# Optimization experiments

Hardware: AMD Instinct MI355X
Metric: run time of the kernel (lower is better)

## Reference

```python
import jax, jax.numpy as jnp
import numpy as np

N_HEADS = 16
HEAD_DIM = 64
ROPE_BASE = 10000.0


def _apply_rope(x, offset):
    # x: (B, T, H, hd); rotates consecutive pairs (x[2i], x[2i+1]) as complex numbers,
    # matching torch.view_as_complex on reshape(..., -1, 2).
    B, T, H, hd = x.shape
    inv_freq = 1.0 / (ROPE_BASE ** (jnp.arange(0, hd, 2, dtype=jnp.float32) / hd))  # (hd/2,)
    t = jnp.arange(T, dtype=jnp.float32) + offset
    ang = t[:, None] * inv_freq[None, :]                      # (T, hd/2)
    cos = jnp.cos(ang)[None, :, None, :]                      # (1, T, 1, hd/2)
    sin = jnp.sin(ang)[None, :, None, :]
    x1 = x[..., 0::2]
    x2 = x[..., 1::2]
    out = jnp.stack([x1 * cos - x2 * sin, x1 * sin + x2 * cos], axis=-1)
    return out.reshape(B, T, H, hd).astype(x.dtype)


def setup_inputs() -> dict:
    key = jax.random.key(0)
    ks = jax.random.split(key, 5)
    D = N_HEADS * HEAD_DIM  # 1024
    s = 1.0 / np.sqrt(D)
    x = jax.random.normal(ks[0], (2, 2048, D), jnp.float32)
    Wqkv = jax.random.normal(ks[1], (D, 3 * D), jnp.float32) * s
    bqkv = jax.random.normal(ks[2], (3 * D,), jnp.float32) * 0.01
    Wout = jax.random.normal(ks[3], (D, D), jnp.float32) * s
    bout = jax.random.normal(ks[4], (D,), jnp.float32) * 0.01
    return {"x": x, "Wqkv": Wqkv, "bqkv": bqkv, "Wout": Wout, "bout": bout, "offset": 0}


def reference(x, Wqkv, bqkv, Wout, bout, offset):
    B, T, D = x.shape
    qkv = (x @ Wqkv + bqkv).reshape(B, T, 3, N_HEADS, HEAD_DIM)
    q, k, v = qkv[:, :, 0], qkv[:, :, 1], qkv[:, :, 2]       # (B, T, H, hd)
    q = _apply_rope(q, offset)
    k = _apply_rope(k, offset)
    # kv_cache is None and T == window_size, so no crop occurs.
    new_cache = jnp.stack([k, v], axis=1)                     # (B, 2, T, H, hd)
    scale = 1.0 / np.sqrt(HEAD_DIM)
    scores = jnp.einsum("bqhd,bkhd->bhqk", q, k) * scale      # (B, H, T, T)
    mask = jnp.tril(jnp.ones((T, T), dtype=bool))
    scores = jnp.where(mask[None, None], scores, jnp.finfo(scores.dtype).min)
    attn = jax.nn.softmax(scores, axis=-1)
    ctx = jnp.einsum("bhqk,bkhd->bqhd", attn, v).reshape(B, T, D)
    out = ctx @ Wout + bout
    return (out, new_cache)
```

## Files before the change

kernel.cpp:

```cpp
#include <hip/hip_runtime.h>
#include <stdint.h>
#include <math.h>


typedef __bf16 bf16_t;
typedef bf16_t bf16x8 __attribute__((ext_vector_type(8)));
typedef float f32x4 __attribute__((ext_vector_type(4)));
typedef unsigned short ushort8_t __attribute__((ext_vector_type(8)));

__device__ __forceinline__ unsigned short f2bf(float f) {
    union { float f; unsigned int i; } v; v.f = f;
    unsigned int r = v.i + 0x7fffu + ((v.i >> 16) & 1u);
    return (unsigned short)(r >> 16);
}
__device__ __forceinline__ bf16x8 ld8(const unsigned short* p) {
    return *(const bf16x8*)p;
}
__device__ __forceinline__ void gload_lds16(const unsigned short* g, unsigned short* l) {
    __builtin_amdgcn_global_load_lds(
        (__attribute__((address_space(1))) void*)(g),
        (__attribute__((address_space(3))) void*)(l),
        16, 0, 0);
}

__global__ void k_cvt(const float* __restrict__ in, unsigned short* __restrict__ out) {
    const int i = (blockIdx.x * 256 + threadIdx.x) * 8;
    float4 a = *(const float4*)&in[i];
    float4 b = *(const float4*)&in[i + 4];
    ushort8_t v;
    v[0] = f2bf(a.x); v[1] = f2bf(a.y); v[2] = f2bf(a.z); v[3] = f2bf(a.w);
    v[4] = f2bf(b.x); v[5] = f2bf(b.y); v[6] = f2bf(b.z); v[7] = f2bf(b.w);
    *(ushort8_t*)&out[i] = v;
}

__global__ void k_ropetab(float* __restrict__ tab, const int* __restrict__ offp) {
    int idx = blockIdx.x * blockDim.x + threadIdx.x;
    int t = idx >> 5, i = idx & 31;
    float off = (float)(*offp);
    float inv = powf(10000.0f, -(float)(2 * i) / 64.0f);
    float ang = ((float)t + off) * inv;
    float s, c;
    sincosf(ang, &s, &c);
    tab[idx * 2]     = c;
    tab[idx * 2 + 1] = s;
}

__global__ void k_transposeF2B(const float* __restrict__ in,
                               unsigned short* __restrict__ out, int R, int C) {
    __shared__ __align__(16) float tile[64 * 68];
    const int bz = blockIdx.z;
    const size_t base = (size_t)bz * R * C;
    const int tR = blockIdx.y * 64, tC = blockIdx.x * 64;
    const int tid = threadIdx.x;
#pragma unroll
    for (int it = 0; it < 4; ++it) {
        int flat = (it * 256 + tid) * 4;
        int r = flat >> 6, c = flat & 63;
        *(float4*)&tile[r * 68 + c] =
            *(const float4*)&in[base + (size_t)(tR + r) * C + tC + c];
    }
    __syncthreads();
#pragma unroll
    for (int it = 0; it < 2; ++it) {
        int flat = (it * 256 + tid) * 8;
        int rr = flat >> 6, cc = flat & 63;
        ushort8_t v;
#pragma unroll
        for (int j = 0; j < 8; ++j) v[j] = f2bf(tile[(cc + j) * 68 + rr]);
        *(ushort8_t*)&out[base + (size_t)(tC + rr) * R + tR + cc] = v;
    }
}

__global__ void k_transpose64(const unsigned short* __restrict__ in,
                              unsigned short* __restrict__ out, int R, int C) {
    __shared__ __align__(16) unsigned short tile[64 * 72];
    const int bz = blockIdx.z;
    const size_t base = (size_t)bz * R * C;
    const int tR = blockIdx.y * 64, tC = blockIdx.x * 64;
    const int tid = threadIdx.x;
#pragma unroll
    for (int it = 0; it < 2; ++it) {
        int flat = (it * 256 + tid) * 8;
        int r = flat >> 6, c = flat & 63;
        *(ushort8_t*)&tile[r * 72 + c] =
            *(const ushort8_t*)&in[base + (size_t)(tR + r) * C + tC + c];
    }
    __syncthreads();
#pragma unroll
    for (int it = 0; it < 2; ++it) {
        int flat = (it * 256 + tid) * 8;
        int rr = flat >> 6, cc = flat & 63;
        ushort8_t v;
#pragma unroll
        for (int j = 0; j < 8; ++j) v[j] = tile[(cc + j) * 72 + rr];
        *(ushort8_t*)&out[base + (size_t)(tC + rr) * R + tR + cc] = v;
    }
}

template <int EPI>
__global__ __launch_bounds__(512, 2) void k_gemm(
    const unsigned short* __restrict__ A,
    const unsigned short* __restrict__ Bt,
    const float* __restrict__ bias,
    const float* __restrict__ tab,
    unsigned short* __restrict__ oq,
    unsigned short* __restrict__ ok,
    unsigned short* __restrict__ ov,
    float* __restrict__ cache,
    float* __restrict__ outp)
{
    constexpr int K = 1024;
    constexpr int NT = 16;
    __shared__ __align__(16) unsigned short lds[65536];
    unsigned short* lA = lds;
    unsigned short* lB = lds + 32768;

    const int tid  = threadIdx.x;
    const int lane = tid & 63, w = tid >> 6;
    const int wr = w >> 2, wc = w & 3;
    const int lrow = lane & 15, quad = lane >> 4;

    const int gx  = gridDim.x;
    const int nwg = gx * gridDim.y;
    const int bid = blockIdx.y * gx + blockIdx.x;
    const int sw  = (bid & 7) * (nwg >> 3) + (bid >> 3);
    const int blockM = (sw / gx) * 256;
    const int blockN = (sw % gx) * 256;

    const int q8    = (lane & 7) ^ (lane >> 3);
    const int srow0 = ((w * 16 + (lane >> 3)) << 1) + ((q8 >> 2) & 1);
    const int scol  = (q8 & 3) * 8;
    const unsigned short* srcA = A  + (size_t)(blockM + srow0) * K + scol;
    const unsigned short* srcB = Bt + (size_t)(blockN + srow0) * K + scol;
    unsigned short* dA = lA + w * 1024;
    unsigned short* dB = lB + w * 1024;

    const int rp   = lrow >> 1;
    const int swzu = ((((lane & 1) << 6) | (quad << 4)) ^ (rp << 4)) >> 1;

    f32x4 acc[8][4];
#pragma unroll
    for (int m = 0; m < 8; ++m)
#pragma unroll
        for (int n = 0; n < 4; ++n) acc[m][n] = (f32x4){0.f, 0.f, 0.f, 0.f};

#define STAGE_A(T, KH) do { \
        const unsigned short* s_ = srcA + (T) * 64 + (KH) * 32; \
        unsigned short* d_ = dA + (((2*(T)+(KH)) & 3) << 13); \
        gload_lds16(s_, d_); \
        gload_lds16(s_ + 16 * K, d_ + 512); } while (0)
#define STAGE_B(T, KH) do { \
        const unsigned short* s_ = srcB + (T) * 64 + (KH) * 32; \
        unsigned short* d_ = dB + (((2*(T)+(KH)) & 3) << 13); \
        gload_lds16(s_, d_); \
        gload_lds16(s_ + 16 * K, d_ + 512); } while (0)

    STAGE_A(0, 0); STAGE_B(0, 0);
    STAGE_A(0, 1); STAGE_B(0, 1);
    STAGE_A(1, 0); STAGE_B(1, 0);
    asm volatile("s_waitcnt vmcnt(8)" ::: "memory");
    __builtin_amdgcn_s_barrier();

    bf16x8 aA[8], bB[2];
    for (int i = 0; i < NT / 2; ++i) {
        const int E = 2 * i, O = 2 * i + 1;
#pragma unroll
        for (int p = 0; p < 8; ++p) {
            const int T    = (p < 4) ? E : O;
            const int ks   = (p >> 1) & 1;
            const int nh   = p & 1;
            const int slot = (2 * T + ks) & 3;
            asm volatile("s_waitcnt vmcnt(6)" ::: "memory");
            if (nh == 0) {
#pragma unroll
                for (int m = 0; m < 8; ++m)
                    aA[m] = ld8(&lA[(slot << 13) + (wr * 64 + m * 8 + rp) * 64 + swzu]);
            }
#pragma unroll
            for (int nl = 0; nl < 2; ++nl)
                bB[nl] = ld8(&lB[(slot << 13) + (wc * 32 + nh * 16 + nl * 8 + rp) * 64 + swzu]);
            if      (p == 0) { STAGE_A(O, 1); }
            else if (p == 1) { STAGE_B(O, 1); }
            else if (p == 2) { if (E + 2 < NT) STAGE_A(E + 2, 0); }
            else if (p == 3) { if (E + 2 < NT) STAGE_B(E + 2, 0); }
            else if (p == 4) { if (E + 2 < NT) STAGE_A(E + 2, 1); }
            else if (p == 5) { if (E + 2 < NT) STAGE_B(E + 2, 1); }
            else if (p == 6) { if (O + 2 < NT) STAGE_A(O + 2, 0); }
            else             { if (O + 2 < NT) STAGE_B(O + 2, 0); }
            __builtin_amdgcn_s_barrier();
            asm volatile("s_waitcnt lgkmcnt(0)" ::: "memory");
            __builtin_amdgcn_sched_barrier(0);
            __builtin_amdgcn_s_setprio(1);
#pragma unroll
            for (int m = 0; m < 8; ++m)
#pragma unroll
                for (int nl = 0; nl < 2; ++nl)
                    acc[m][nh * 2 + nl] = __builtin_amdgcn_mfma_f32_16x16x32_bf16(
                        aA[m], bB[nl], acc[m][nh * 2 + nl], 0, 0, 0);
            __builtin_amdgcn_s_setprio(0);
            __builtin_amdgcn_s_barrier();
        }
    }
#undef STAGE_A
#undef STAGE_B

#pragma unroll
    for (int m = 0; m < 8; ++m) {
        const int rbase = blockM + wr * 128 + m * 16 + quad * 4;
#pragma unroll
        for (int n = 0; n < 4; ++n) {
            const int gcol = blockN + wc * 64 + n * 16 + lrow;
            const float bv = bias[gcol];
#pragma unroll
            for (int r = 0; r < 4; ++r) {
                const int row = rbase + r;
                float val = acc[m][n][r] + bv;
                if (EPI == 0) {
                    outp[(size_t)row * 1024 + gcol] = val;
                } else {
                    const int s = gcol >> 10;
                    const int cn = gcol & 1023;
                    const int h = cn >> 6, d = cn & 63;
                    const int b = row >> 11, t = row & 2047;
                    if (s < 2) {
                        const int ii = d >> 1;
                        const float cz = tab[t * 64 + 2 * ii];
                        const float sz = tab[t * 64 + 2 * ii + 1];
                        const float pv = __shfl_xor(val, 1);
                        val = (d & 1) ? (pv * sz + val * cz) : (val * cz - pv * sz);
                    }
                    const unsigned short r16 = f2bf(val);
                    const size_t bhtd = (((size_t)(b * 16 + h)) * 2048 + t) * 64 + d;
                    if (s == 0) {
                        oq[bhtd] = r16;
                    } else if (s == 1) {
                        ok[bhtd] = r16;
                        cache[(((size_t)(b * 2 + 0)) * 2048 + t) * 1024 + h * 64 + d] = val;
                    } else {
                        ov[bhtd] = r16;
                        cache[(((size_t)(b * 2 + 1)) * 2048 + t) * 1024 + h * 64 + d] = val;
                    }
                }
            }
        }
    }
}

__global__ __launch_bounds__(256, 3) void k_attn(
    const unsigned short* __restrict__ qh,
    const unsigned short* __restrict__ kh,
    const unsigned short* __restrict__ vt,
    unsigned short* __restrict__ ctx)
{
    __shared__ __align__(16) unsigned short lK[2][64 * 64];
    __shared__ __align__(16) unsigned short lV[2][64 * 64];
    __shared__ __align__(16) unsigned short lP[4][32 * 68];
    const int tid = threadIdx.x;
    const int wave = tid >> 6, lane = tid & 63;
    const int lrow = lane & 15, quad = lane >> 4;
    const int sub = lane >> 3, g8 = lane & 7;
    const int grp = g8 ^ (sub & 7);
    const int pj = blockIdx.x;
    const int h = blockIdx.y, b = blockIdx.z;
    const unsigned short* Q  = qh + (size_t)(b * 16 + h) * 2048 * 64;
    const unsigned short* Kp = kh + (size_t)(b * 16 + h) * 2048 * 64;
    const unsigned short* Vt = vt + (size_t)(b * 16 + h) * 64 * 2048;

    bf16x8 bOnes;
#pragma unroll
    for (int j = 0; j < 8; ++j) bOnes[j] = (bf16_t)1.0f;

    for (int phase = 0; phase < 2; ++phase) {
        const int qb = phase ? pj : (15 - pj);
        const int qw = qb * 128 + wave * 32;

        bf16x8 aQ[2][2];
#pragma unroll
        for (int mf = 0; mf < 2; ++mf)
#pragma unroll
            for (int ks = 0; ks < 2; ++ks) {
                bf16x8 t = ld8(&Q[(size_t)(qw + mf * 16 + lrow) * 64 + ks * 32 + quad * 8]);
#pragma unroll
                for (int j = 0; j < 8; ++j) t[j] = (bf16_t)((float)t[j] * 0.125f);
                aQ[mf][ks] = t;
            }

        f32x4 o[2][4];
#pragma unroll
        for (int mf = 0; mf < 2; ++mf)
#pragma unroll
            for (int i = 0; i < 4; ++i) o[mf][i] = (f32x4){0.f, 0.f, 0.f, 0.f};
        f32x4 lacc[2];
        lacc[0] = (f32x4){0.f, 0.f, 0.f, 0.f};
        lacc[1] = (f32x4){0.f, 0.f, 0.f, 0.f};

        const int nT = 2 * (qb + 1);

        __syncthreads();
#pragma unroll
        for (int i = 0; i < 2; ++i) {
            const int c = wave * 2 + i;
            gload_lds16(&Kp[(size_t)(c * 8 + sub) * 64 + grp * 8], &lK[0][c * 512]);
            gload_lds16(&Vt[(size_t)(c * 8 + sub) * 2048 + grp * 8], &lV[0][c * 512]);
        }

        int buf = 0;
        for (int it = 0; it < nT; ++it) {
            const int kt0 = it * 64;
            __syncthreads();
            if (it + 1 < nT) {
                const int kn = kt0 + 64;
#pragma unroll
                for (int i = 0; i < 2; ++i) {
                    const int c = wave * 2 + i;
                    gload_lds16(&Kp[(size_t)(kn + c * 8 + sub) * 64 + grp * 8], &lK[buf ^ 1][c * 512]);
                    gload_lds16(&Vt[(size_t)(c * 8 + sub) * 2048 + kn + grp * 8], &lV[buf ^ 1][c * 512]);
                }
            }
            if (kt0 < qw + 32) {
                const unsigned short* lKb = lK[buf];
                const unsigned short* lVb = lV[buf];
                f32x4 s[2][4];
#pragma unroll
                for (int mf = 0; mf < 2; ++mf)
#pragma unroll
                    for (int i = 0; i < 4; ++i) s[mf][i] = (f32x4){0.f, 0.f, 0.f, 0.f};
#pragma unroll
                for (int nt = 0; nt < 4; ++nt) {
                    const int row = nt * 16 + lrow;
#pragma unroll
                    for (int ks = 0; ks < 2; ++ks) {
                        bf16x8 bK = ld8(&lKb[row * 64 + (((ks * 4 + quad) ^ (row & 7)) * 8)]);
#pragma unroll
                        for (int mf = 0; mf < 2; ++mf)
                            s[mf][nt] = __builtin_amdgcn_mfma_f32_16x16x32_bf16(
                                aQ[mf][ks], bK, s[mf][nt], 0, 0, 0);
                    }
                }
                if (kt0 + 63 > qw) {
#pragma unroll
                    for (int mf = 0; mf < 2; ++mf)
#pragma unroll
                        for (int nt = 0; nt < 4; ++nt) {
                            const int colg = kt0 + nt * 16 + lrow;
#pragma unroll
                            for (int r = 0; r < 4; ++r) {
                                const int rowg = qw + mf * 16 + quad * 4 + r;
                                const float pv = (colg <= rowg) ? __expf(s[mf][nt][r]) : 0.f;
                                lP[wave][(mf * 16 + quad * 4 + r) * 68 + nt * 16 + lrow] = f2bf(pv);
                            }
                        }
                } else {
#pragma unroll
                    for (int mf = 0; mf < 2; ++mf)
#pragma unroll
                        for (int nt = 0; nt < 4; ++nt)
#pragma unroll
                            for (int r = 0; r < 4; ++r)
                                lP[wave][(mf * 16 + quad * 4 + r) * 68 + nt * 16 + lrow] =
                                    f2bf(__expf(s[mf][nt][r]));
                }
                bf16x8 aP[2][2];
#pragma unroll
                for (int mf = 0; mf < 2; ++mf)
#pragma unroll
                    for (int ks = 0; ks < 2; ++ks)
                        aP[mf][ks] = ld8(&lP[wave][(mf * 16 + lrow) * 68 + ks * 32 + quad * 8]);
#pragma unroll
                for (int mf = 0; mf < 2; ++mf)
#pragma unroll
                    for (int ks = 0; ks < 2; ++ks)
                        lacc[mf] = __builtin_amdgcn_mfma_f32_16x16x32_bf16(
                            aP[mf][ks], bOnes, lacc[mf], 0, 0, 0);
#pragma unroll
                for (int dt = 0; dt < 4; ++dt) {
                    const int row = dt * 16 + lrow;
#pragma unroll
                    for (int ks = 0; ks < 2; ++ks) {
                        bf16x8 bV = ld8(&lVb[row * 64 + (((ks * 4 + quad) ^ (row & 7)) * 8)]);
#pragma unroll
                        for (int mf = 0; mf < 2; ++mf)
                            o[mf][dt] = __builtin_amdgcn_mfma_f32_16x16x32_bf16(
                                aP[mf][ks], bV, o[mf][dt], 0, 0, 0);
                    }
                }
            }
            buf ^= 1;
        }

        float inv[2][4];
#pragma unroll
        for (int mf = 0; mf < 2; ++mf)
#pragma unroll
            for (int r = 0; r < 4; ++r) inv[mf][r] = 1.0f / lacc[mf][r];
#pragma unroll
        for (int mf = 0; mf < 2; ++mf)
#pragma unroll
            for (int dt = 0; dt < 4; ++dt) {
                const int col = h * 64 + dt * 16 + lrow;
#pragma unroll
                for (int r = 0; r < 4; ++r) {
                    const int trow = qw + mf * 16 + quad * 4 + r;
                    ctx[((size_t)(b * 2048 + trow)) * 1024 + col] = f2bf(o[mf][dt][r] * inv[mf][r]);
                }
            }
    }
}

extern "C" void kernel_launch(void* const* d_in, const int* in_sizes, int n_in,
                              void* d_out, int out_size, void* d_ws, size_t ws_size,
                              hipStream_t stream) {
    (void)in_sizes; (void)n_in; (void)out_size; (void)ws_size;
    const float* x    = (const float*)d_in[0];
    const float* wqkv = (const float*)d_in[1];
    const float* bqkv = (const float*)d_in[2];
    const float* wout = (const float*)d_in[3];
    const float* bout = (const float*)d_in[4];
    const int*   offp = (const int*)d_in[5];

    float* out   = (float*)d_out;
    float* cache = out + (size_t)2 * 2048 * 1024;

    char* w = (char*)d_ws;
    float* tab            = (float*)w;          w += (size_t)2048 * 64 * sizeof(float);
    unsigned short* xb    = (unsigned short*)w; w += (size_t)4194304 * 2;
    unsigned short* wqkvT = (unsigned short*)w; w += (size_t)3072 * 1024 * 2;
    unsigned short* woutT = (unsigned short*)w; w += (size_t)1024 * 1024 * 2;
    unsigned short* qh    = (unsigned short*)w; w += (size_t)4194304 * 2;
    unsigned short* kh    = (unsigned short*)w; w += (size_t)4194304 * 2;
    unsigned short* vh    = (unsigned short*)w; w += (size_t)4194304 * 2;
    unsigned short* vt    = (unsigned short*)w; w += (size_t)4194304 * 2;
    unsigned short* ctx   = (unsigned short*)w; w += (size_t)4194304 * 2;

    k_ropetab<<<dim3(256), dim3(256), 0, stream>>>(tab, offp);
    k_cvt<<<dim3(2048), dim3(256), 0, stream>>>(x, xb);
    k_transposeF2B<<<dim3(48, 16, 1), dim3(256), 0, stream>>>(wqkv, wqkvT, 1024, 3072);
    k_transposeF2B<<<dim3(16, 16, 1), dim3(256), 0, stream>>>(wout, woutT, 1024, 1024);
    k_gemm<1><<<dim3(12, 16), dim3(512), 0, stream>>>(xb, wqkvT, bqkv, tab, qh, kh, vh, cache, nullptr);
    k_transpose64<<<dim3(1, 32, 32), dim3(256), 0, stream>>>(vh, vt, 2048, 64);
    k_attn<<<dim3(8, 16, 2), dim3(256), 0, stream>>>(qh, kh, vt, ctx);
    k_gemm<0><<<dim3(4, 16), dim3(512), 0, stream>>>(ctx, woutT, bout, tab, nullptr, nullptr, nullptr, nullptr, out);
}
```

Baseline: 258.1 us.

## Run both causal attention phases concurrently and manually unroll GEMM pipeline

The attention kernel now launches 512 threads per block, and each group of four waves handles one of the two paired query blocks at the same time instead of running the two phases one after the other. K/V tiles are loaded once and shared by both groups. The GEMM main loop is unrolled by hand with an explicit prologue and epilogue, which drops the per-stage conditionals and tail checks. The attention change adds work imbalance, since one group finishes early and idles, and it raises register and LDS pressure.

```diff
diff --git a/kernel.cpp b/kernel.cpp
--- a/kernel.cpp
+++ b/kernel.cpp
@@ -110,7 +110,6 @@
     float* __restrict__ outp)
 {
     constexpr int K = 1024;
-    constexpr int NT = 16;
     __shared__ __align__(16) unsigned short lds[65536];
     unsigned short* lA = lds;
     unsigned short* lB = lds + 32768;
@@ -154,55 +153,60 @@
         unsigned short* d_ = dB + (((2*(T)+(KH)) & 3) << 13); \
         gload_lds16(s_, d_); \
         gload_lds16(s_ + 16 * K, d_ + 512); } while (0)
+#define WAITN(n) asm volatile("s_waitcnt vmcnt(" #n ")" ::: "memory")
+#define RD_A(slot) do { \
+        _Pragma("unroll") \
+        for (int m = 0; m < 8; ++m) \
+            aA[m] = ld8(&lA[((slot) << 13) + (wr * 64 + m * 8 + rp) * 64 + swzu]); } while (0)
+#define RD_B(slot, nh) do { \
+        _Pragma("unroll") \
+        for (int nl = 0; nl < 2; ++nl) \
+            bB[nl] = ld8(&lB[((slot) << 13) + (wc * 32 + (nh) * 16 + nl * 8 + rp) * 64 + swzu]); } while (0)
+#define MFMA16(nh) do { \
+        __builtin_amdgcn_s_barrier(); \
+        asm volatile("s_waitcnt lgkmcnt(0)" ::: "memory"); \
+        __builtin_amdgcn_sched_barrier(0); \
+        __builtin_amdgcn_s_setprio(1); \
+        _Pragma("unroll") \
+        for (int m = 0; m < 8; ++m) { \
+            acc[m][(nh)*2+0] = __builtin_amdgcn_mfma_f32_16x16x32_bf16(aA[m], bB[0], acc[m][(nh)*2+0], 0, 0, 0); \
+            acc[m][(nh)*2+1] = __builtin_amdgcn_mfma_f32_16x16x32_bf16(aA[m], bB[1], acc[m][(nh)*2+1], 0, 0, 0); } \
+        __builtin_amdgcn_s_setprio(0); \
+        __builtin_amdgcn_s_barrier(); } while (0)
 
     STAGE_A(0, 0); STAGE_B(0, 0);
     STAGE_A(0, 1); STAGE_B(0, 1);
     STAGE_A(1, 0); STAGE_B(1, 0);
+    STAGE_A(1, 1);
     asm volatile("s_waitcnt vmcnt(8)" ::: "memory");
     __builtin_amdgcn_s_barrier();
 
     bf16x8 aA[8], bB[2];
-    for (int i = 0; i < NT / 2; ++i) {
+    for (int i = 0; i < 7; ++i) {
         const int E = 2 * i, O = 2 * i + 1;
-#pragma unroll
-        for (int p = 0; p < 8; ++p) {
-            const int T    = (p < 4) ? E : O;
-            const int ks   = (p >> 1) & 1;
-            const int nh   = p & 1;
-            const int slot = (2 * T + ks) & 3;
-            asm volatile("s_waitcnt vmcnt(6)" ::: "memory");
-            if (nh == 0) {
-#pragma unroll
-                for (int m = 0; m < 8; ++m)
-                    aA[m] = ld8(&lA[(slot << 13) + (wr * 64 + m * 8 + rp) * 64 + swzu]);
-            }
-#pragma unroll
-            for (int nl = 0; nl < 2; ++nl)
-                bB[nl] = ld8(&lB[(slot << 13) + (wc * 32 + nh * 16 + nl * 8 + rp) * 64 + swzu]);
-            if      (p == 0) { STAGE_A(O, 1); }
-            else if (p == 1) { STAGE_B(O, 1); }
-            else if (p == 2) { if (E + 2 < NT) STAGE_A(E + 2, 0); }
-            else if (p == 3) { if (E + 2 < NT) STAGE_B(E + 2, 0); }
-            else if (p == 4) { if (E + 2 < NT) STAGE_A(E + 2, 1); }
-            else if (p == 5) { if (E + 2 < NT) STAGE_B(E + 2, 1); }
-            else if (p == 6) { if (O + 2 < NT) STAGE_A(O + 2, 0); }
-            else             { if (O + 2 < NT) STAGE_B(O + 2, 0); }
-            __builtin_amdgcn_s_barrier();
-            asm volatile("s_waitcnt lgkmcnt(0)" ::: "memory");
-            __builtin_amdgcn_sched_barrier(0);
-            __builtin_amdgcn_s_setprio(1);
-#pragma unroll
-            for (int m = 0; m < 8; ++m)
-#pragma unroll
-                for (int nl = 0; nl < 2; ++nl)
-                    acc[m][nh * 2 + nl] = __builtin_amdgcn_mfma_f32_16x16x32_bf16(
-                        aA[m], bB[nl], acc[m][nh * 2 + nl], 0, 0, 0);
-            __builtin_amdgcn_s_setprio(0);
-            __builtin_amdgcn_s_barrier();
-        }
-    }
+        WAITN(6); RD_A(0); RD_B(0, 0); STAGE_B(O, 1);     MFMA16(0);
+        RD_B(0, 1);                    STAGE_A(E + 2, 0); MFMA16(1);
+        WAITN(6); RD_A(1); RD_B(1, 0); STAGE_B(E + 2, 0); MFMA16(0);
+        RD_B(1, 1);                    STAGE_A(E + 2, 1); MFMA16(1);
+        WAITN(6); RD_A(2); RD_B(2, 0); STAGE_B(E + 2, 1); MFMA16(0);
+        RD_B(2, 1);                    STAGE_A(O + 2, 0); MFMA16(1);
+        WAITN(6); RD_A(3); RD_B(3, 0); STAGE_B(O + 2, 0); MFMA16(0);
+        RD_B(3, 1);                    STAGE_A(O + 2, 1); MFMA16(1);
+    }
+    WAITN(6); RD_A(0); RD_B(0, 0); STAGE_B(15, 1); MFMA16(0);
+    RD_B(0, 1);                                    MFMA16(1);
+    WAITN(2); RD_A(1); RD_B(1, 0);                 MFMA16(0);
+    RD_B(1, 1);                                    MFMA16(1);
+    WAITN(0); RD_A(2); RD_B(2, 0);                 MFMA16(0);
+    RD_B(2, 1);                                    MFMA16(1);
+    RD_A(3); RD_B(3, 0);                           MFMA16(0);
+    RD_B(3, 1);                                    MFMA16(1);
 #undef STAGE_A
 #undef STAGE_B
+#undef WAITN
+#undef RD_A
+#undef RD_B
+#undef MFMA16
 
 #pragma unroll
     for (int m = 0; m < 8; ++m) {
@@ -246,7 +250,7 @@
     }
 }
 
-__global__ __launch_bounds__(256, 3) void k_attn(
+__global__ __launch_bounds__(512, 2) void k_attn(
     const unsigned short* __restrict__ qh,
     const unsigned short* __restrict__ kh,
     const unsigned short* __restrict__ vt,
@@ -254,7 +258,7 @@
 {
     __shared__ __align__(16) unsigned short lK[2][64 * 64];
     __shared__ __align__(16) unsigned short lV[2][64 * 64];
-    __shared__ __align__(16) unsigned short lP[4][32 * 68];
+    __shared__ __align__(16) unsigned short lP[8][32 * 68];
     const int tid = threadIdx.x;
     const int wave = tid >> 6, lane = tid & 63;
     const int lrow = lane & 15, quad = lane >> 4;
@@ -266,145 +270,139 @@
     const unsigned short* Kp = kh + (size_t)(b * 16 + h) * 2048 * 64;
     const unsigned short* Vt = vt + (size_t)(b * 16 + h) * 64 * 2048;
 
+    const int grpq = wave >> 2;
+    const int wv   = wave & 3;
+    const int qb   = grpq ? pj : (15 - pj);
+    const int qw   = qb * 128 + wv * 32;
+    const int nT   = 2 * (16 - pj);
+
     bf16x8 bOnes;
 #pragma unroll
     for (int j = 0; j < 8; ++j) bOnes[j] = (bf16_t)1.0f;
 
-    for (int phase = 0; phase < 2; ++phase) {
-        const int qb = phase ? pj : (15 - pj);
-        const int qw = qb * 128 + wave * 32;
-
-        bf16x8 aQ[2][2];
-#pragma unroll
-        for (int mf = 0; mf < 2; ++mf)
-#pragma unroll
-            for (int ks = 0; ks < 2; ++ks) {
-                bf16x8 t = ld8(&Q[(size_t)(qw + mf * 16 + lrow) * 64 + ks * 32 + quad * 8]);
-#pragma unroll
-                for (int j = 0; j < 8; ++j) t[j] = (bf16_t)((float)t[j] * 0.125f);
-                aQ[mf][ks] = t;
-            }
-
-        f32x4 o[2][4];
-#pragma unroll
-        for (int mf = 0; mf < 2; ++mf)
-#pragma unroll
-            for (int i = 0; i < 4; ++i) o[mf][i] = (f32x4){0.f, 0.f, 0.f, 0.f};
-        f32x4 lacc[2];
-        lacc[0] = (f32x4){0.f, 0.f, 0.f, 0.f};
-        lacc[1] = (f32x4){0.f, 0.f, 0.f, 0.f};
-
-        const int nT = 2 * (qb + 1);
-
+    bf16x8 aQ[2][2];
+#pragma unroll
+    for (int mf = 0; mf < 2; ++mf)
+#pragma unroll
+        for (int ks = 0; ks < 2; ++ks) {
+            bf16x8 t = ld8(&Q[(size_t)(qw + mf * 16 + lrow) * 64 + ks * 32 + quad * 8]);
+#pragma unroll
+            for (int j = 0; j < 8; ++j) t[j] = (bf16_t)((float)t[j] * 0.125f);
+            aQ[mf][ks] = t;
+        }
+
+    f32x4 o[2][4];
+#pragma unroll
+    for (int mf = 0; mf < 2; ++mf)
+#pragma unroll
+        for (int i = 0; i < 4; ++i) o[mf][i] = (f32x4){0.f, 0.f, 0.f, 0.f};
+    f32x4 lacc[2];
+    lacc[0] = (f32x4){0.f, 0.f, 0.f, 0.f};
+    lacc[1] = (f32x4){0.f, 0.f, 0.f, 0.f};
+
+    {
+        const int c = wave;
+        gload_lds16(&Kp[(size_t)(c * 8 + sub) * 64 + grp * 8], &lK[0][c * 512]);
+        gload_lds16(&Vt[(size_t)(c * 8 + sub) * 2048 + grp * 8], &lV[0][c * 512]);
+    }
+
+    int buf = 0;
+    for (int it = 0; it < nT; ++it) {
+        const int kt0 = it * 64;
         __syncthreads();
-#pragma unroll
-        for (int i = 0; i < 2; ++i) {
-            const int c = wave * 2 + i;
-            gload_lds16(&Kp[(size_t)(c * 8 + sub) * 64 + grp * 8], &lK[0][c * 512]);
-            gload_lds16(&Vt[(size_t)(c * 8 + sub) * 2048 + grp * 8], &lV[0][c * 512]);
+        if (it + 1 < nT) {
+            const int kn = kt0 + 64;
+            const int c = wave;
+            gload_lds16(&Kp[(size_t)(kn + c * 8 + sub) * 64 + grp * 8], &lK[buf ^ 1][c * 512]);
+            gload_lds16(&Vt[(size_t)(c * 8 + sub) * 2048 + kn + grp * 8], &lV[buf ^ 1][c * 512]);
         }
-
-        int buf = 0;
-        for (int it = 0; it < nT; ++it) {
-            const int kt0 = it * 64;
-            __syncthreads();
-            if (it + 1 < nT) {
-                const int kn = kt0 + 64;
-#pragma unroll
-                for (int i = 0; i < 2; ++i) {
-                    const int c = wave * 2 + i;
-                    gload_lds16(&Kp[(size_t)(kn + c * 8 + sub) * 64 + grp * 8], &lK[buf ^ 1][c * 512]);
-                    gload_lds16(&Vt[(size_t)(c * 8 + sub) * 2048 + kn + grp * 8], &lV[buf ^ 1][c * 512]);
+        if (kt0 < qw + 32) {
+            const unsigned short* lKb = lK[buf];
+            const unsigned short* lVb = lV[buf];
+            f32x4 s[2][4];
+#pragma unroll
+            for (int mf = 0; mf < 2; ++mf)
+#pragma unroll
+                for (int i = 0; i < 4; ++i) s[mf][i] = (f32x4){0.f, 0.f, 0.f, 0.f};
+#pragma unroll
+            for (int nt = 0; nt < 4; ++nt) {
+                const int row = nt * 16 + lrow;
+#pragma unroll
+                for (int ks = 0; ks < 2; ++ks) {
+                    bf16x8 bK = ld8(&lKb[row * 64 + (((ks * 4 + quad) ^ (row & 7)) * 8)]);
+#pragma unroll
+                    for (int mf = 0; mf < 2; ++mf)
+                        s[mf][nt] = __builtin_amdgcn_mfma_f32_16x16x32_bf16(
+                            aQ[mf][ks], bK, s[mf][nt], 0, 0, 0);
                 }
             }
-            if (kt0 < qw + 32) {
-                const unsigned short* lKb = lK[buf];
-                const unsigned short* lVb = lV[buf];
-                f32x4 s[2][4];
+            if (kt0 + 63 > qw) {
 #pragma unroll
                 for (int mf = 0; mf < 2; ++mf)
 #pragma unroll
-                    for (int i = 0; i < 4; ++i) s[mf][i] = (f32x4){0.f, 0.f, 0.f, 0.f};
-#pragma unroll
-                for (int nt = 0; nt < 4; ++nt) {
-                    const int row = nt * 16 + lrow;
-#pragma unroll
-                    for (int ks = 0; ks < 2; ++ks) {
-                        bf16x8 bK = ld8(&lKb[row * 64 + (((ks * 4 + quad) ^ (row & 7)) * 8)]);
-#pragma unroll
-                        for (int mf = 0; mf < 2; ++mf)
-                            s[mf][nt] = __builtin_amdgcn_mfma_f32_16x16x32_bf16(
-                                aQ[mf][ks], bK, s[mf][nt], 0, 0, 0);
+                    for (int nt = 0; nt < 4; ++nt) {
+                        const int colg = kt0 + nt * 16 + lrow;
+#pragma unroll
+                        for (int r = 0; r < 4; ++r) {
+                            const int rowg = qw + mf * 16 + quad * 4 + r;
+                            const float pv = (colg <= rowg) ? __expf(s[mf][nt][r]) : 0.f;
+                            lP[wave][(mf * 16 + quad * 4 + r) * 68 + nt * 16 + lrow] = f2bf(pv);
+                        }
                     }
-                }
-                if (kt0 + 63 > qw) {
+            } else {
+#pragma unroll
+                for (int mf = 0; mf < 2; ++mf)
+#pragma unroll
+                    for (int nt = 0; nt < 4; ++nt)
+#pragma unroll
+                        for (int r = 0; r < 4; ++r)
+                            lP[wave][(mf * 16 + quad * 4 + r) * 68 + nt * 16 + lrow] =
+                                f2bf(__expf(s[mf][nt][r]));
+            }
+            bf16x8 aP[2][2];
+#pragma unroll
+            for (int mf = 0; mf < 2; ++mf)
+#pragma unroll
+                for (int ks = 0; ks < 2; ++ks)
+                    aP[mf][ks] = ld8(&lP[wave][(mf * 16 + lrow) * 68 + ks * 32 + quad * 8]);
+#pragma unroll
+            for (int mf = 0; mf < 2; ++mf)
+#pragma unroll
+                for (int ks = 0; ks < 2; ++ks)
+                    lacc[mf] = __builtin_amdgcn_mfma_f32_16x16x32_bf16(
+                        aP[mf][ks], bOnes, lacc[mf], 0, 0, 0);
+#pragma unroll
+            for (int dt = 0; dt < 4; ++dt) {
+                const int row = dt * 16 + lrow;
+#pragma unroll
+                for (int ks = 0; ks < 2; ++ks) {
+                    bf16x8 bV = ld8(&lVb[row * 64 + (((ks * 4 + quad) ^ (row & 7)) * 8)]);
 #pragma unroll
                     for (int mf = 0; mf < 2; ++mf)
-#pragma unroll
-                        for (int nt = 0; nt < 4; ++nt) {
-                            const int colg = kt0 + nt * 16 + lrow;
-#pragma unroll
-                            for (int r = 0; r < 4; ++r) {
-                                const int rowg = qw + mf * 16 + quad * 4 + r;
-                                const float pv = (colg <= rowg) ? __expf(s[mf][nt][r]) : 0.f;
-                                lP[wave][(mf * 16 + quad * 4 + r) * 68 + nt * 16 + lrow] = f2bf(pv);
-                            }
-                        }
-                } else {
-#pragma unroll
-                    for (int mf = 0; mf < 2; ++mf)
-#pragma unroll
-                        for (int nt = 0; nt < 4; ++nt)
-#pragma unroll
-                            for (int r = 0; r < 4; ++r)
-                                lP[wave][(mf * 16 + quad * 4 + r) * 68 + nt * 16 + lrow] =
-                                    f2bf(__expf(s[mf][nt][r]));
-                }
-                bf16x8 aP[2][2];
-#pragma unroll
-                for (int mf = 0; mf < 2; ++mf)
-#pragma unroll
-                    for (int ks = 0; ks < 2; ++ks)
-                        aP[mf][ks] = ld8(&lP[wave][(mf * 16 + lrow) * 68 + ks * 32 + quad * 8]);
-#pragma unroll
-                for (int mf = 0; mf < 2; ++mf)
-#pragma unroll
-                    for (int ks = 0; ks < 2; ++ks)
-                        lacc[mf] = __builtin_amdgcn_mfma_f32_16x16x32_bf16(
-                            aP[mf][ks], bOnes, lacc[mf], 0, 0, 0);
-#pragma unroll
-                for (int dt = 0; dt < 4; ++dt) {
-                    const int row = dt * 16 + lrow;
-#pragma unroll
-                    for (int ks = 0; ks < 2; ++ks) {
-                        bf16x8 bV = ld8(&lVb[row * 64 + (((ks * 4 + quad) ^ (row & 7)) * 8)]);
-#pragma unroll
-                        for (int mf = 0; mf < 2; ++mf)
-                            o[mf][dt] = __builtin_amdgcn_mfma_f32_16x16x32_bf16(
-                                aP[mf][ks], bV, o[mf][dt], 0, 0, 0);
-                    }
+                        o[mf][dt] = __builtin_amdgcn_mfma_f32_16x16x32_bf16(
+                            aP[mf][ks], bV, o[mf][dt], 0, 0, 0);
                 }
             }
-            buf ^= 1;
         }
-
-        float inv[2][4];
-#pragma unroll
-        for (int mf = 0; mf < 2; ++mf)
-#pragma unroll
-            for (int r = 0; r < 4; ++r) inv[mf][r] = 1.0f / lacc[mf][r];
-#pragma unroll
-        for (int mf = 0; mf < 2; ++mf)
-#pragma unroll
-            for (int dt = 0; dt < 4; ++dt) {
-                const int col = h * 64 + dt * 16 + lrow;
-#pragma unroll
-                for (int r = 0; r < 4; ++r) {
-                    const int trow = qw + mf * 16 + quad * 4 + r;
-                    ctx[((size_t)(b * 2048 + trow)) * 1024 + col] = f2bf(o[mf][dt][r] * inv[mf][r]);
-                }
+        buf ^= 1;
+    }
+
+    float inv[2][4];
+#pragma unroll
+    for (int mf = 0; mf < 2; ++mf)
+#pragma unroll
+        for (int r = 0; r < 4; ++r) inv[mf][r] = 1.0f / lacc[mf][r];
+#pragma unroll
+    for (int mf = 0; mf < 2; ++mf)
+#pragma unroll
+        for (int dt = 0; dt < 4; ++dt) {
+            const int col = h * 64 + dt * 16 + lrow;
+#pragma unroll
+            for (int r = 0; r < 4; ++r) {
+                const int trow = qw + mf * 16 + quad * 4 + r;
+                ctx[((size_t)(b * 2048 + trow)) * 1024 + col] = f2bf(o[mf][dt][r] * inv[mf][r]);
             }
-    }
+        }
 }
 
 extern "C" void kernel_launch(void* const* d_in, const int* in_sizes, int n_in,
@@ -438,6 +436,6 @@
     k_transposeF2B<<<dim3(16, 16, 1), dim3(256), 0, stream>>>(wout, woutT, 1024, 1024);
     k_gemm<1><<<dim3(12, 16), dim3(512), 0, stream>>>(xb, wqkvT, bqkv, tab, qh, kh, vh, cache, nullptr);
     k_transpose64<<<dim3(1, 32, 32), dim3(256), 0, stream>>>(vh, vt, 2048, 64);
-    k_attn<<<dim3(8, 16, 2), dim3(256), 0, stream>>>(qh, kh, vt, ctx);
+    k_attn<<<dim3(8, 16, 2), dim3(512), 0, stream>>>(qh, kh, vt, ctx);
     k_gemm<0><<<dim3(4, 16), dim3(512), 0, stream>>>(ctx, woutT, bout, tab, nullptr, nullptr, nullptr, nullptr, out);
 }
```

Result: no change. 256.4 us (-0.7%).
